# Kernel tuning notes

Measured on AMD Instinct MI355X. Metric: run time of the kernel, lower is better.

Reference implementation:

```python
import jax, jax.numpy as jnp
import numpy as np

B, T, C = 2, 2048, 2048
NH, NG, HS = 16, 4, 128      # heads, query groups, head size
DCONV = 4                    # causal conv kernel width
IM = 5632                    # MLP intermediate size
EPS = 1e-5


def rmsnorm(x, w):
    return x * jax.lax.rsqrt(jnp.mean(x * x, axis=-1, keepdims=True) + EPS) * w


def causal_conv_silu(x, w):
    # x: (B, T, D), w: (D, kw) depthwise; left-pad kw-1 -> causal, then SiLU
    xt = jnp.transpose(x, (0, 2, 1))  # (B, D, T)
    y = jax.lax.conv_general_dilated(
        xt, w[:, None, :], window_strides=(1,), padding=[(DCONV - 1, 0)],
        dimension_numbers=('NCH', 'OIH', 'NCH'), feature_group_count=w.shape[0])
    return jnp.transpose(jax.nn.silu(y), (0, 2, 1))


def apply_rope(x, cos, sin):
    # flash-attn non-interleaved: rotate halves of the rotary dim
    d = cos.shape[-1]
    x1, x2 = x[..., :d], x[..., d:2 * d]
    c = cos[None, :, None, :]
    s = sin[None, :, None, :]
    return jnp.concatenate([x1 * c - x2 * s, x1 * s + x2 * c], axis=-1)


def setup_inputs() -> dict:
    key = jax.random.key(0)
    ks = jax.random.split(key, 12)
    sc = 0.02
    pos = jnp.arange(T, dtype=jnp.float32)
    inv_freq = 1.0 / (10000.0 ** (jnp.arange(0, HS // 2, dtype=jnp.float32) / (HS // 2)))
    ang = pos[:, None] * inv_freq[None, :]  # (T, HS/2)
    return {
        'x': jax.random.normal(ks[0], (B, T, C), jnp.float32),
        'cos': jnp.cos(ang), 'sin': jnp.sin(ang),
        'norm1_w': jnp.ones((C,), jnp.float32),
        'attn_w': jax.random.normal(ks[1], ((NH + 2 * NG) * HS, C), jnp.float32) * sc,
        'proj_w': jax.random.normal(ks[2], (C, C), jnp.float32) * sc,
        'qconv_w': jax.random.normal(ks[3], (NH * HS, DCONV), jnp.float32) * 0.2,
        'kconv_w': jax.random.normal(ks[4], (NG * HS, DCONV), jnp.float32) * 0.2,
        'vconv_w': jax.random.normal(ks[5], (NG * HS, DCONV), jnp.float32) * 0.2,
        'norm2_w': jnp.ones((C,), jnp.float32),
        'fc1_w': jax.random.normal(ks[6], (IM, C), jnp.float32) * sc,
        'fc2_w': jax.random.normal(ks[7], (IM, C), jnp.float32) * sc,
        'mlp_proj_w': jax.random.normal(ks[8], (C, IM), jnp.float32) * sc,
    }


def reference(x, cos, sin, norm1_w, attn_w, proj_w, qconv_w, kconv_w, vconv_w,
              norm2_w, fc1_w, fc2_w, mlp_proj_w):
    q_per_kv = NH // NG
    n1 = rmsnorm(x, norm1_w)
    qkv = n1 @ attn_w.T                                   # (B,T,(NH+2NG)*HS)
    qkv = qkv.reshape(B, T, NG, q_per_kv + 2, HS)
    q = qkv[:, :, :, :q_per_kv].reshape(B, T, -1)         # (B,T,NH*HS)
    k = qkv[:, :, :, q_per_kv:q_per_kv + 1].reshape(B, T, -1)
    v = qkv[:, :, :, q_per_kv + 1:].reshape(B, T, -1)
    # short depthwise causal conv + silu (sc_attn)
    q = causal_conv_silu(q, qconv_w)
    k = causal_conv_silu(k, kconv_w)
    v = causal_conv_silu(v, vconv_w)
    q = q.reshape(B, T, NH, HS)
    k = k.reshape(B, T, NG, HS)
    v = v.reshape(B, T, NG, HS)
    q = apply_rope(q, cos, sin)
    k = apply_rope(k, cos, sin)
    # GQA: repeat kv groups to match heads
    k = jnp.repeat(k, q_per_kv, axis=2)
    v = jnp.repeat(v, q_per_kv, axis=2)
    scale = 1.0 / np.sqrt(HS)
    scores = jnp.einsum('bthd,bshd->bhts', q, k) * scale  # (B,NH,T,T)
    causal = jnp.tril(jnp.ones((T, T), bool))
    scores = jnp.where(causal[None, None], scores, jnp.finfo(scores.dtype).min)
    att = jax.nn.softmax(scores, axis=-1)
    y = jnp.einsum('bhts,bshd->bthd', att, v).reshape(B, T, C)
    x = x + y @ proj_w.T                                  # attn residual
    n2 = rmsnorm(x, norm2_w)
    mlp = (jax.nn.silu(n2 @ fc1_w.T) * (n2 @ fc2_w.T)) @ mlp_proj_w.T
    return x + mlp
```

## Files before the change

### kernel.cpp

```cpp
#include <hip/hip_runtime.h>
#include <hip/hip_bf16.h>
#include <stdint.h>

#define DEV static __device__ __forceinline__

typedef unsigned short ushort_t;
typedef __attribute__((ext_vector_type(8))) short bf16x8;
typedef __attribute__((ext_vector_type(8))) short short8;
typedef __attribute__((ext_vector_type(4))) float f32x4;

DEV ushort_t f2bf(float f) {
  union { float f; unsigned u; } v; v.f = f;
  unsigned r = v.u + 0x7FFFu + ((v.u >> 16) & 1u);
  return (ushort_t)(r >> 16);
}

DEV void async16(const void* g, void* l) {
  __builtin_amdgcn_global_load_lds((const __attribute__((address_space(1))) void*)g,
                                   (__attribute__((address_space(3))) void*)l,
                                   16, 0, 0);
}

__global__ __launch_bounds__(256) void k_cvt(const float* __restrict__ in,
                                             ushort_t* __restrict__ out, int n) {
  int i = (blockIdx.x * 256 + threadIdx.x) * 4;
  if (i >= n) return;
  float4 v = *(const float4*)(in + i);
  ushort4 o = { f2bf(v.x), f2bf(v.y), f2bf(v.z), f2bf(v.w) };
  *(ushort4*)(out + i) = o;
}

__global__ __launch_bounds__(256) void k_rmsnorm(const float* __restrict__ x,
                                                 const float* __restrict__ w,
                                                 ushort_t* __restrict__ out) {
  __shared__ float red[4];
  int row = blockIdx.x, tid = threadIdx.x;
  const float* xr = x + (size_t)row * 2048 + tid * 8;
  float4 a = *(const float4*)xr;
  float4 b = *(const float4*)(xr + 4);
  float s = a.x*a.x + a.y*a.y + a.z*a.z + a.w*a.w
          + b.x*b.x + b.y*b.y + b.z*b.z + b.w*b.w;
#pragma unroll
  for (int m = 1; m < 64; m <<= 1) s += __shfl_xor(s, m);
  if ((tid & 63) == 0) red[tid >> 6] = s;
  __syncthreads();
  float inv = rsqrtf((red[0] + red[1] + red[2] + red[3]) * (1.0f / 2048.0f) + 1e-5f);
  const float* wp = w + tid * 8;
  ushort_t* op = out + (size_t)row * 2048 + tid * 8;
  ushort4 o0 = { f2bf(a.x*inv*wp[0]), f2bf(a.y*inv*wp[1]), f2bf(a.z*inv*wp[2]), f2bf(a.w*inv*wp[3]) };
  ushort4 o1 = { f2bf(b.x*inv*wp[4]), f2bf(b.y*inv*wp[5]), f2bf(b.z*inv*wp[6]), f2bf(b.w*inv*wp[7]) };
  *(ushort4*)op = o0;
  *(ushort4*)(op + 4) = o1;
}

template<int KIND>
__global__ __launch_bounds__(256) void k_convrope(const float* __restrict__ qkv,
                                                  const float* __restrict__ cw,
                                                  const float* __restrict__ cs,
                                                  const float* __restrict__ sn,
                                                  ushort_t* __restrict__ outp) {
  const int H = (KIND == 0) ? 16 : 4;
  size_t gid = (size_t)blockIdx.x * 256 + threadIdx.x;
  int i = (int)(gid & 63);
  size_t r = gid >> 6;
  int t = (int)(r & 2047); r >>= 11;
  int h = (int)(r % H);
  int b = (int)(r / H);
  int col0;
  if (KIND == 0)      col0 = (h >> 2) * 768 + (h & 3) * 128;
  else if (KIND == 1) col0 = h * 768 + 512;
  else                col0 = h * 768 + 640;
  const float* w1 = cw + (h * 128 + i) * 4;
  const float* w2 = cw + (h * 128 + 64 + i) * 4;
  float x1 = 0.f, x2 = 0.f;
#pragma unroll
  for (int j = 0; j < 4; j++) {
    int tj = t - 3 + j;
    if (tj >= 0) {
      const float* rp = qkv + ((size_t)b * 2048 + tj) * 3072 + col0 + i;
      x1 += w1[j] * rp[0];
      x2 += w2[j] * rp[64];
    }
  }
  x1 = x1 / (1.f + __expf(-x1));
  x2 = x2 / (1.f + __expf(-x2));
  float o1 = x1, o2 = x2;
  if (KIND != 2) {
    float c = cs[t * 64 + i], s = sn[t * 64 + i];
    o1 = x1 * c - x2 * s;
    o2 = x1 * s + x2 * c;
  }
  ushort_t* o = outp + (((size_t)b * H + h) * 2048 + t) * 128;
  o[i] = f2bf(o1);
  o[i + 64] = f2bf(o2);
}

__global__ __launch_bounds__(256) void k_transpose(const ushort_t* __restrict__ v,
                                                   ushort_t* __restrict__ vt) {
  __shared__ ushort_t tile[64][72];
  int bg = blockIdx.z;
  int t0 = blockIdx.x * 64;
  int d0 = blockIdx.y * 64;
  int r = threadIdx.x >> 2, c0 = (threadIdx.x & 3) * 16;
  const ushort_t* src = v + ((size_t)bg * 2048 + t0) * 128 + d0 + (size_t)r * 128 + c0;
  *(short8*)&tile[r][c0]     = *(const short8*)src;
  *(short8*)&tile[r][c0 + 8] = *(const short8*)(src + 8);
  __syncthreads();
  short8 a, b2;
#pragma unroll
  for (int j = 0; j < 8; j++) {
    a[j]  = (short)tile[c0 + j][r];
    b2[j] = (short)tile[c0 + 8 + j][r];
  }
  ushort_t* dst = vt + ((size_t)bg * 128 + d0 + r) * 2048 + t0 + c0;
  *(short8*)dst       = a;
  *(short8*)(dst + 8) = b2;
}

#define EPI_F32 0
#define EPI_ADD 1
#define EPI_SILUMUL 2
#define EPI_BF16 3

template<int EPI>
__global__ __launch_bounds__(256) void k_gemm(const ushort_t* __restrict__ A,
                                              const ushort_t* __restrict__ B,
                                              int M, int N, int K,
                                              const float* __restrict__ Rf,
                                              const ushort_t* __restrict__ Rb,
                                              float* __restrict__ outf,
                                              ushort_t* __restrict__ outb) {
  __shared__ ushort_t As[128 * 64];
  __shared__ ushort_t Bs[128 * 64];
  int tid = threadIdx.x, lane = tid & 63, wid = tid >> 6;
  int wr = wid >> 1, wc = wid & 1;
  int nbn = N >> 7;
  int mb = blockIdx.x / nbn, nb = blockIdx.x % nbn;
  const ushort_t* Ab = A + (size_t)mb * 128 * K;
  const ushort_t* Bb = B + (size_t)nb * 128 * K;
  f32x4 acc[4][4] = {};
  for (int k0 = 0; k0 < K; k0 += 64) {
    __syncthreads();
#pragma unroll
    for (int c = 0; c < 4; c++) {
      int o = c * 4096 + tid * 16;
      int row = o >> 7;
      int src = (o & 127) ^ ((row & 7) << 4);
      int ldso = (c * 4096 + wid * 1024) >> 1;
      async16(Ab + (size_t)row * K + k0 + (src >> 1), As + ldso);
      async16(Bb + (size_t)row * K + k0 + (src >> 1), Bs + ldso);
    }
    __syncthreads();
#pragma unroll
    for (int ks = 0; ks < 2; ks++) {
      bf16x8 af[4], bfr[4];
#pragma unroll
      for (int i = 0; i < 4; i++) {
        int ra = wr * 64 + i * 16 + (lane & 15);
        int byt = ks * 64 + ((lane >> 4) << 4);
        af[i] = *(const bf16x8*)((const char*)As + ra * 128 + (byt ^ ((ra & 7) << 4)));
        int rb = wc * 64 + i * 16 + (lane & 15);
        bfr[i] = *(const bf16x8*)((const char*)Bs + rb * 128 + (byt ^ ((rb & 7) << 4)));
      }
#pragma unroll
      for (int i = 0; i < 4; i++)
#pragma unroll
        for (int j = 0; j < 4; j++)
          acc[i][j] = __builtin_amdgcn_mfma_f32_16x16x32_bf16(af[i], bfr[j], acc[i][j], 0, 0, 0);
    }
  }
  int g = lane >> 4, cl = lane & 15;
#pragma unroll
  for (int i = 0; i < 4; i++)
#pragma unroll
    for (int j = 0; j < 4; j++)
#pragma unroll
      for (int rr = 0; rr < 4; rr++) {
        int rowg = mb * 128 + wr * 64 + i * 16 + g * 4 + rr;
        int colg = nb * 128 + wc * 64 + j * 16 + cl;
        size_t idx = (size_t)rowg * N + colg;
        float v = acc[i][j][rr];
        if (EPI == EPI_F32) {
          outf[idx] = v;
        } else if (EPI == EPI_ADD) {
          outf[idx] = v + Rf[idx];
        } else if (EPI == EPI_SILUMUL) {
          float a = __bfloat162float(*(const __hip_bfloat16*)&Rb[idx]);
          outb[idx] = f2bf((a / (1.f + __expf(-a))) * v);
        } else {
          outb[idx] = f2bf(v);
        }
      }
}

__global__ __launch_bounds__(256) void k_attn(const ushort_t* __restrict__ Q,
                                              const ushort_t* __restrict__ Kk,
                                              const ushort_t* __restrict__ VT,
                                              ushort_t* __restrict__ Y) {
  __shared__ ushort_t Ks[64 * 128];
  __shared__ ushort_t Vt[128 * 64];
  __shared__ ushort_t Ps[4 * 16 * 64];
  int qt = 31 - (int)blockIdx.x;
  int h = blockIdx.y, b = blockIdx.z, g = h >> 2;
  int tid = threadIdx.x, lane = tid & 63, w = tid >> 6;
  const ushort_t* Qg  = Q  + (((size_t)b * 16 + h) * 2048 + (size_t)qt * 64) * 128;
  const ushort_t* Kg  = Kk + ((size_t)b * 4 + g) * 2048 * 128;
  const ushort_t* VTg = VT + ((size_t)b * 4 + g) * 128 * 2048;
#pragma unroll
  for (int c = 0; c < 4; c++) {
    int o = c * 4096 + tid * 16;
    int row = o >> 8;
    int src = (o & 255) ^ ((row & 7) << 4);
    async16(Qg + row * 128 + (src >> 1), Ks + ((c * 4096 + w * 1024) >> 1));
  }
  __syncthreads();
  bf16x8 qf[4];
#pragma unroll
  for (int k = 0; k < 4; k++) {
    int row = w * 16 + (lane & 15);
    int byt = k * 64 + ((lane >> 4) << 4);
    qf[k] = *(const bf16x8*)((const char*)Ks + row * 256 + (byt ^ ((row & 7) << 4)));
  }
  f32x4 oacc[8] = {};
  float mrow[4], lrow[4];
#pragma unroll
  for (int rr = 0; rr < 4; rr++) { mrow[rr] = -1e30f; lrow[rr] = 0.f; }
  ushort_t* Pw = Ps + w * 16 * 64;
  for (int kv = 0; kv <= qt; kv++) {
    __syncthreads();
    const ushort_t* Kt = Kg + (size_t)kv * 64 * 128;
#pragma unroll
    for (int c = 0; c < 4; c++) {
      int o = c * 4096 + tid * 16;
      int row = o >> 8;
      int src = (o & 255) ^ ((row & 7) << 4);
      async16(Kt + row * 128 + (src >> 1), Ks + ((c * 4096 + w * 1024) >> 1));
    }
#pragma unroll
    for (int c = 0; c < 4; c++) {
      int o = c * 4096 + tid * 16;
      int row = o >> 7;
      int src = (o & 127) ^ ((row & 7) << 4);
      async16(VTg + (size_t)row * 2048 + kv * 64 + (src >> 1), Vt + ((c * 4096 + w * 1024) >> 1));
    }
    __syncthreads();
    f32x4 sacc[4] = {};
#pragma unroll
    for (int n = 0; n < 4; n++)
#pragma unroll
      for (int k = 0; k < 4; k++) {
        int row = n * 16 + (lane & 15);
        int byt = k * 64 + ((lane >> 4) << 4);
        bf16x8 kf = *(const bf16x8*)((const char*)Ks + row * 256 + (byt ^ ((row & 7) << 4)));
        sacc[n] = __builtin_amdgcn_mfma_f32_16x16x32_bf16(qf[k], kf, sacc[n], 0, 0, 0);
      }
    const float scl = 0.08838834764831845f;
    float corr[4];
#pragma unroll
    for (int rr = 0; rr < 4; rr++) {
      float mx = -1e30f;
#pragma unroll
      for (int n = 0; n < 4; n++) {
        float s = sacc[n][rr] * scl;
        if (kv == qt) {
          int qrow = w * 16 + (lane >> 4) * 4 + rr;
          int kcol = n * 16 + (lane & 15);
          if (kcol > qrow) s = -1e30f;
        }
        sacc[n][rr] = s;
        mx = fmaxf(mx, s);
      }
      mx = fmaxf(mx, __shfl_xor(mx, 1));
      mx = fmaxf(mx, __shfl_xor(mx, 2));
      mx = fmaxf(mx, __shfl_xor(mx, 4));
      mx = fmaxf(mx, __shfl_xor(mx, 8));
      float mnew = fmaxf(mrow[rr], mx);
      float co = __expf(mrow[rr] - mnew);
      mrow[rr] = mnew;
      corr[rr] = co;
      float ps = 0.f;
#pragma unroll
      for (int n = 0; n < 4; n++) {
        float p = __expf(sacc[n][rr] - mnew);
        sacc[n][rr] = p;
        ps += p;
      }
      lrow[rr] = lrow[rr] * co + ps;
    }
#pragma unroll
    for (int no = 0; no < 8; no++)
#pragma unroll
      for (int rr = 0; rr < 4; rr++) oacc[no][rr] *= corr[rr];
#pragma unroll
    for (int n = 0; n < 4; n++)
#pragma unroll
      for (int rr = 0; rr < 4; rr++) {
        int prow = (lane >> 4) * 4 + rr;
        int pbyt = (n * 16 + (lane & 15)) * 2;
        *(ushort_t*)((char*)Pw + prow * 128 + (pbyt ^ ((prow & 7) << 4))) = f2bf(sacc[n][rr]);
      }
    asm volatile("s_waitcnt lgkmcnt(0)" ::: "memory");
    __builtin_amdgcn_sched_barrier(0);
#pragma unroll
    for (int ks = 0; ks < 2; ks++) {
      int prow = lane & 15;
      int pbyt = ks * 64 + ((lane >> 4) << 4);
      bf16x8 pf = *(const bf16x8*)((const char*)Pw + prow * 128 + (pbyt ^ ((prow & 7) << 4)));
#pragma unroll
      for (int no = 0; no < 8; no++) {
        int vrow = no * 16 + (lane & 15);
        bf16x8 vf = *(const bf16x8*)((const char*)Vt + vrow * 128 + (pbyt ^ ((vrow & 7) << 4)));
        oacc[no] = __builtin_amdgcn_mfma_f32_16x16x32_bf16(pf, vf, oacc[no], 0, 0, 0);
      }
    }
  }
  float inv[4];
#pragma unroll
  for (int rr = 0; rr < 4; rr++) {
    float s = lrow[rr];
    s += __shfl_xor(s, 1);
    s += __shfl_xor(s, 2);
    s += __shfl_xor(s, 4);
    s += __shfl_xor(s, 8);
    inv[rr] = 1.f / s;
  }
#pragma unroll
  for (int no = 0; no < 8; no++)
#pragma unroll
    for (int rr = 0; rr < 4; rr++) {
      int t = qt * 64 + w * 16 + (lane >> 4) * 4 + rr;
      int col = no * 16 + (lane & 15);
      Y[((size_t)b * 2048 + t) * 2048 + h * 128 + col] = f2bf(oacc[no][rr] * inv[rr]);
    }
}

extern "C" void kernel_launch(void* const* d_in, const int* in_sizes, int n_in,
                              void* d_out, int out_size, void* d_ws, size_t ws_size,
                              hipStream_t stream) {
  (void)in_sizes; (void)n_in; (void)out_size; (void)ws_size;
  const float* x     = (const float*)d_in[0];
  const float* cosp  = (const float*)d_in[1];
  const float* sinp  = (const float*)d_in[2];
  const float* n1w   = (const float*)d_in[3];
  const float* attnw = (const float*)d_in[4];
  const float* projw = (const float*)d_in[5];
  const float* qcw   = (const float*)d_in[6];
  const float* kcw   = (const float*)d_in[7];
  const float* vcw   = (const float*)d_in[8];
  const float* n2w   = (const float*)d_in[9];
  const float* fc1w  = (const float*)d_in[10];
  const float* fc2w  = (const float*)d_in[11];
  const float* mlpw  = (const float*)d_in[12];
  float* outp = (float*)d_out;

  char* p = (char*)d_ws;
  ushort_t* attn_bf = (ushort_t*)p; p += (size_t)3072 * 2048 * 2;
  ushort_t* proj_bf = (ushort_t*)p; p += (size_t)2048 * 2048 * 2;
  ushort_t* fc1_bf  = (ushort_t*)p; p += (size_t)5632 * 2048 * 2;
  ushort_t* fc2_bf  = (ushort_t*)p; p += (size_t)5632 * 2048 * 2;
  ushort_t* mlp_bf  = (ushort_t*)p; p += (size_t)2048 * 5632 * 2;
  ushort_t* n_bf    = (ushort_t*)p; p += (size_t)4096 * 2048 * 2;
  char* bufA = p; p += (size_t)4096 * 3072 * 4;
  char* bufB = p; p += (size_t)4096 * 5632 * 2;

  float*    qkv_f = (float*)bufA;
  ushort_t* vt_bf = (ushort_t*)bufA;
  ushort_t* a_bf  = (ushort_t*)bufA;
  ushort_t* q_bf  = (ushort_t*)bufB;
  ushort_t* k_bf  = (ushort_t*)(bufB + (size_t)16777216);
  ushort_t* v_bf  = (ushort_t*)(bufB + (size_t)20971520);
  ushort_t* y_bf  = (ushort_t*)(bufB + (size_t)25165824);
  ushort_t* h_bf  = (ushort_t*)bufB;

  k_cvt<<<3072 * 2048 / 1024, 256, 0, stream>>>(attnw, attn_bf, 3072 * 2048);
  k_cvt<<<2048 * 2048 / 1024, 256, 0, stream>>>(projw, proj_bf, 2048 * 2048);
  k_cvt<<<5632 * 2048 / 1024, 256, 0, stream>>>(fc1w, fc1_bf, 5632 * 2048);
  k_cvt<<<5632 * 2048 / 1024, 256, 0, stream>>>(fc2w, fc2_bf, 5632 * 2048);
  k_cvt<<<2048 * 5632 / 1024, 256, 0, stream>>>(mlpw, mlp_bf, 2048 * 5632);

  k_rmsnorm<<<4096, 256, 0, stream>>>(x, n1w, n_bf);

  k_gemm<EPI_F32><<<32 * 24, 256, 0, stream>>>(n_bf, attn_bf, 4096, 3072, 2048,
                                               nullptr, nullptr, qkv_f, nullptr);

  k_convrope<0><<<16384, 256, 0, stream>>>(qkv_f, qcw, cosp, sinp, q_bf);
  k_convrope<1><<<4096, 256, 0, stream>>>(qkv_f, kcw, cosp, sinp, k_bf);
  k_convrope<2><<<4096, 256, 0, stream>>>(qkv_f, vcw, cosp, sinp, v_bf);

  k_transpose<<<dim3(32, 2, 8), 256, 0, stream>>>(v_bf, vt_bf);

  k_attn<<<dim3(32, 16, 2), 256, 0, stream>>>(q_bf, k_bf, vt_bf, y_bf);

  k_gemm<EPI_ADD><<<32 * 16, 256, 0, stream>>>(y_bf, proj_bf, 4096, 2048, 2048,
                                               x, nullptr, outp, nullptr);

  k_rmsnorm<<<4096, 256, 0, stream>>>(outp, n2w, n_bf);

  k_gemm<EPI_BF16><<<32 * 44, 256, 0, stream>>>(n_bf, fc1_bf, 4096, 5632, 2048,
                                                nullptr, nullptr, nullptr, a_bf);
  k_gemm<EPI_SILUMUL><<<32 * 44, 256, 0, stream>>>(n_bf, fc2_bf, 4096, 5632, 2048,
                                                   nullptr, a_bf, nullptr, h_bf);
  k_gemm<EPI_ADD><<<32 * 16, 256, 0, stream>>>(h_bf, mlp_bf, 4096, 2048, 5632,
                                               outp, nullptr, outp, nullptr);
}
```

Measured before the change: 970.3 us.

## Double-buffer GEMM LDS tiles and split MFMA into two phases

The GEMM kernel now uses two LDS buffers per operand, so the async global-to-LDS load for the next K tile is issued before the current tile is computed. This hides global load latency behind the MFMA work, where before each step waited on a full load. The compute step is split into two half-row phases, with barriers, s_setprio raised around the MFMA bursts, and launch bounds set to two blocks per CU. The cost is double the LDS use (64 KB per block), which may limit occupancy, plus extra barriers per tile.

```diff
diff --git a/kernel.cpp b/kernel.cpp
--- a/kernel.cpp
+++ b/kernel.cpp
@@ -122,51 +122,83 @@
 #define EPI_SILUMUL 2
 #define EPI_BF16 3
 
+DEV void stage_tile(const ushort_t* Ab, const ushort_t* Bb, int K, int k0,
+                    ushort_t* As, ushort_t* Bs, int tid) {
+#pragma unroll
+  for (int c = 0; c < 4; c++) {
+    int o = c * 4096 + tid * 16;
+    int row = o >> 7;
+    int src = (o & 127) ^ ((row & 7) << 4);
+    int ldso = (c * 4096 + (tid >> 6) * 1024) >> 1;
+    async16(Ab + (size_t)row * K + k0 + (src >> 1), As + ldso);
+    async16(Bb + (size_t)row * K + k0 + (src >> 1), Bs + ldso);
+  }
+}
+
 template<int EPI>
-__global__ __launch_bounds__(256) void k_gemm(const ushort_t* __restrict__ A,
-                                              const ushort_t* __restrict__ B,
-                                              int M, int N, int K,
-                                              const float* __restrict__ Rf,
-                                              const ushort_t* __restrict__ Rb,
-                                              float* __restrict__ outf,
-                                              ushort_t* __restrict__ outb) {
-  __shared__ ushort_t As[128 * 64];
-  __shared__ ushort_t Bs[128 * 64];
-  int tid = threadIdx.x, lane = tid & 63, wid = tid >> 6;
+__global__ __launch_bounds__(256, 2) void k_gemm(const ushort_t* __restrict__ A,
+                                                 const ushort_t* __restrict__ B,
+                                                 int M, int N, int K,
+                                                 const float* __restrict__ Rf,
+                                                 const ushort_t* __restrict__ Rb,
+                                                 float* __restrict__ outf,
+                                                 ushort_t* __restrict__ outb) {
+  __shared__ ushort_t As[2][128 * 64];
+  __shared__ ushort_t Bs[2][128 * 64];
+  int tid = threadIdx.x, lane = tid & 63;
+  int wid = tid >> 6;
   int wr = wid >> 1, wc = wid & 1;
   int nbn = N >> 7;
   int mb = blockIdx.x / nbn, nb = blockIdx.x % nbn;
   const ushort_t* Ab = A + (size_t)mb * 128 * K;
   const ushort_t* Bb = B + (size_t)nb * 128 * K;
   f32x4 acc[4][4] = {};
-  for (int k0 = 0; k0 < K; k0 += 64) {
-    __syncthreads();
-#pragma unroll
-    for (int c = 0; c < 4; c++) {
-      int o = c * 4096 + tid * 16;
-      int row = o >> 7;
-      int src = (o & 127) ^ ((row & 7) << 4);
-      int ldso = (c * 4096 + wid * 1024) >> 1;
-      async16(Ab + (size_t)row * K + k0 + (src >> 1), As + ldso);
-      async16(Bb + (size_t)row * K + k0 + (src >> 1), Bs + ldso);
-    }
-    __syncthreads();
-#pragma unroll
-    for (int ks = 0; ks < 2; ks++) {
-      bf16x8 af[4], bfr[4];
-#pragma unroll
-      for (int i = 0; i < 4; i++) {
-        int ra = wr * 64 + i * 16 + (lane & 15);
-        int byt = ks * 64 + ((lane >> 4) << 4);
-        af[i] = *(const bf16x8*)((const char*)As + ra * 128 + (byt ^ ((ra & 7) << 4)));
-        int rb = wc * 64 + i * 16 + (lane & 15);
-        bfr[i] = *(const bf16x8*)((const char*)Bs + rb * 128 + (byt ^ ((rb & 7) << 4)));
-      }
-#pragma unroll
-      for (int i = 0; i < 4; i++)
-#pragma unroll
-        for (int j = 0; j < 4; j++)
-          acc[i][j] = __builtin_amdgcn_mfma_f32_16x16x32_bf16(af[i], bfr[j], acc[i][j], 0, 0, 0);
+  int nt = K >> 6;
+  stage_tile(Ab, Bb, K, 0, As[0], Bs[0], tid);
+  asm volatile("s_waitcnt vmcnt(0)" ::: "memory");
+  __builtin_amdgcn_s_barrier();
+  for (int t = 0; t < nt; ++t) {
+    int cur = t & 1;
+    if (t + 1 < nt)
+      stage_tile(Ab, Bb, K, (t + 1) << 6, As[cur ^ 1], Bs[cur ^ 1], tid);
+#pragma unroll
+    for (int ph = 0; ph < 2; ++ph) {
+      bf16x8 af[2][2], bfr[4][2];
+#pragma unroll
+      for (int r = 0; r < 2; ++r)
+#pragma unroll
+        for (int kk = 0; kk < 2; ++kk) {
+          int ra = wr * 64 + (ph * 2 + r) * 16 + (lane & 15);
+          int byt = kk * 64 + ((lane >> 4) << 4);
+          af[r][kk] = *(const bf16x8*)((const char*)As[cur] + ra * 128 + (byt ^ ((ra & 7) << 4)));
+        }
+#pragma unroll
+      for (int j = 0; j < 4; ++j)
+#pragma unroll
+        for (int kk = 0; kk < 2; ++kk) {
+          int rb = wc * 64 + j * 16 + (lane & 15);
+          int byt = kk * 64 + ((lane >> 4) << 4);
+          bfr[j][kk] = *(const bf16x8*)((const char*)Bs[cur] + rb * 128 + (byt ^ ((rb & 7) << 4)));
+        }
+      __builtin_amdgcn_s_barrier();
+      asm volatile("s_waitcnt lgkmcnt(0)" ::: "memory");
+      __builtin_amdgcn_sched_barrier(0);
+      __builtin_amdgcn_s_setprio(1);
+#pragma unroll
+      for (int r = 0; r < 2; ++r)
+#pragma unroll
+        for (int j = 0; j < 4; ++j)
+#pragma unroll
+          for (int kk = 0; kk < 2; ++kk)
+            acc[ph * 2 + r][j] = __builtin_amdgcn_mfma_f32_16x16x32_bf16(
+                af[r][kk], bfr[j][kk], acc[ph * 2 + r][j], 0, 0, 0);
+      __builtin_amdgcn_s_setprio(0);
+      if (ph == 0) {
+        __builtin_amdgcn_s_barrier();
+      } else {
+        asm volatile("s_waitcnt vmcnt(0)" ::: "memory");
+        __builtin_amdgcn_s_barrier();
+      }
     }
   }
   int g = lane >> 4, cl = lane & 15;
```

After: 970.8 us. About the same (+0.1%).
